# Kernel optimization log

Measured on AMD Instinct MI355X. Metric: run time of the kernel, lower is better.

Reference implementation:

```python
import jax, jax.numpy as jnp
import numpy as np

N = 50000       # nodes
E = 800000      # edges (before self loops)
F_IN = 128      # feat_dim
H = 8           # heads
C = 64          # hidden_dim (per-head out_channels, averaged since concat=False)
G = 64          # graphs in batch
NEG_SLOPE = 0.2


def setup_inputs() -> dict:
    key = jax.random.key(0)
    ks = jax.random.split(key, 16)
    inp = {
        "x": jax.random.normal(ks[0], (N, F_IN), jnp.float32),
        "edge_index": jax.random.randint(ks[1], (2, E), 0, N, dtype=jnp.int32),
        "batch": jnp.sort(jax.random.randint(ks[2], (N,), 0, G, dtype=jnp.int32)),
        "edge_attr": jax.random.normal(ks[3], (E, 4), jnp.float32),
    }
    # GATConv params per layer: lin weight [in, H*C], att_src/att_dst [H, C], bias [C]
    dims_in = [F_IN, C, C]
    for i, din in enumerate(dims_in):
        s = 1.0 / np.sqrt(din)
        inp[f"W{i}"] = jax.random.uniform(ks[4 + 3 * i], (din, H * C), jnp.float32, -s, s)
        inp[f"asrc{i}"] = jax.random.uniform(ks[5 + 3 * i], (H, C), jnp.float32, -s, s)
        inp[f"adst{i}"] = jax.random.uniform(ks[6 + 3 * i], (H, C), jnp.float32, -s, s)
        inp[f"b{i}"] = jnp.zeros((C,), jnp.float32)
    return inp


def _gat_conv(x, src, dst, W, asrc, adst, b):
    n = x.shape[0]
    h = (x @ W).reshape(n, H, C)                       # [N,H,C]
    a_s = (h * asrc[None]).sum(-1)                     # [N,H]
    a_d = (h * adst[None]).sum(-1)                     # [N,H]
    e = a_s[src] + a_d[dst]                            # [Etot,H]
    e = jnp.where(e > 0, e, NEG_SLOPE * e)             # leaky_relu(0.2)
    # segment softmax over incoming edges of each dst node (self loops => nonempty)
    m = jax.ops.segment_max(e, dst, num_segments=n)    # [N,H]
    ex = jnp.exp(e - m[dst])
    denom = jax.ops.segment_sum(ex, dst, num_segments=n)
    alpha = ex / denom[dst]                            # [Etot,H]
    out = jax.ops.segment_sum(alpha[:, :, None] * h[src], dst, num_segments=n)  # [N,H,C]
    return out.mean(axis=1) + b[None]                  # concat=False -> head mean, + bias


def reference(x, edge_index, batch, edge_attr,
              W0, asrc0, adst0, b0,
              W1, asrc1, adst1, b1,
              W2, asrc2, adst2, b2):
    # edge_attr is ignored: GATConv built without edge_dim has no lin_edge.
    loop = jnp.arange(N, dtype=edge_index.dtype)
    src = jnp.concatenate([edge_index[0], loop])       # PyG add_self_loops=True
    dst = jnp.concatenate([edge_index[1], loop])
    layers = [(W0, asrc0, adst0, b0), (W1, asrc1, adst1, b1), (W2, asrc2, adst2, b2)]
    xs = []
    h = x
    for (W, a_s, a_d, b) in layers:
        h = jax.nn.elu(_gat_conv(h, src, dst, W, a_s, a_d, b))
        xs.append(h)
    # pool='sum' -> global_add_pool per layer, then concat over layers
    pooled = [jax.ops.segment_sum(t, batch, num_segments=G) for t in xs]
    global_rep = jnp.concatenate(pooled, axis=1)       # [G, 3*C]
    return global_rep, h
```

## Files before the change

### kernel.cpp

```cpp
#include <hip/hip_runtime.h>
#include <math.h>

#define NN 50000
#define EE 800000
#define ET (EE + NN)
#define FIN 128
#define HH 8
#define CC 64
#define HC 512
#define HU 256
#define GG 64
#define POOL_SZ (GG * 3 * CC)

typedef short short8 __attribute__((ext_vector_type(8)));
typedef float floatx4 __attribute__((ext_vector_type(4)));

__device__ __forceinline__ unsigned bf16pack(float a, float b) {
    unsigned ua = __float_as_uint(a), ub = __float_as_uint(b);
    ua = (ua + 0x7FFFu + ((ua >> 16) & 1u)) >> 16;
    ub = (ub + 0x7FFFu + ((ub >> 16) & 1u)) >> 16;
    return ua | (ub << 16);
}
__device__ __forceinline__ unsigned short bf16r(float a) {
    unsigned ua = __float_as_uint(a);
    return (unsigned short)((ua + 0x7FFFu + ((ua >> 16) & 1u)) >> 16);
}
__device__ __forceinline__ float bf_lo(unsigned u) { return __uint_as_float(u << 16); }
__device__ __forceinline__ float bf_hi(unsigned u) { return __uint_as_float(u & 0xFFFF0000u); }


__global__ void k_cvt(const float* __restrict__ in, unsigned* __restrict__ out, int n8) {
    int i = blockIdx.x * blockDim.x + threadIdx.x;
    if (i < n8) {
        float4 a = ((const float4*)in)[i * 2];
        float4 b = ((const float4*)in)[i * 2 + 1];
        uint4 o;
        o.x = bf16pack(a.x, a.y); o.y = bf16pack(a.z, a.w);
        o.z = bf16pack(b.x, b.y); o.w = bf16pack(b.z, b.w);
        ((uint4*)out)[i] = o;
    }
}


__global__ void k_init(int* cnt) {
    int i = blockIdx.x * blockDim.x + threadIdx.x;
    if (i < NN) cnt[i] = 1;
}

__global__ void k_count(const int* __restrict__ dst, int* cnt) {
    int e = blockIdx.x * blockDim.x + threadIdx.x;
    if (e < EE) atomicAdd(&cnt[dst[e]], 1);
}

#define SCAN_B 256
__global__ void k_scan1(const int* __restrict__ cnt, int* off, int* bsum, int n) {
    __shared__ int s[SCAN_B];
    int i = blockIdx.x * SCAN_B + threadIdx.x;
    int v = (i < n) ? cnt[i] : 0;
    s[threadIdx.x] = v;
    __syncthreads();
    for (int d = 1; d < SCAN_B; d <<= 1) {
        int t = (threadIdx.x >= d) ? s[threadIdx.x - d] : 0;
        __syncthreads();
        s[threadIdx.x] += t;
        __syncthreads();
    }
    if (i < n) off[i] = s[threadIdx.x] - v;
    if (threadIdx.x == SCAN_B - 1) bsum[blockIdx.x] = s[SCAN_B - 1];
}

__global__ void k_scan2(int* bsum, int nb) {
    __shared__ int s[SCAN_B];
    int v = (threadIdx.x < nb) ? bsum[threadIdx.x] : 0;
    s[threadIdx.x] = v;
    __syncthreads();
    for (int d = 1; d < SCAN_B; d <<= 1) {
        int t = (threadIdx.x >= d) ? s[threadIdx.x - d] : 0;
        __syncthreads();
        s[threadIdx.x] += t;
        __syncthreads();
    }
    if (threadIdx.x < nb) bsum[threadIdx.x] = s[threadIdx.x] - v;
}

__global__ void k_scan3(int* off, const int* __restrict__ bsum, int* cursor, int n, int total) {
    int i = blockIdx.x * blockDim.x + threadIdx.x;
    if (i < n) {
        int v = off[i] + bsum[i / SCAN_B];
        off[i] = v;
        cursor[i] = v + 1;
    }
    if (i == 0) off[n] = total;
}

__global__ void k_fillself(const int* __restrict__ off, int* col) {
    int i = blockIdx.x * blockDim.x + threadIdx.x;
    if (i < NN) col[off[i]] = i;
}

__global__ void k_fill(const int* __restrict__ src, const int* __restrict__ dst,
                       int* cursor, int* col) {
    int e = blockIdx.x * blockDim.x + threadIdx.x;
    if (e < EE) {
        int p = atomicAdd(&cursor[dst[e]], 1);
        col[p] = src[e];
    }
}


template<int K>
__global__ __launch_bounds__(256) void k_gemm_mfma(
        const unsigned short* __restrict__ A,
        const float* __restrict__ W,
        const float* __restrict__ asrc, const float* __restrict__ adst,
        unsigned short* __restrict__ hout,
        float* __restrict__ as_out, float* __restrict__ ad_out, int M) {
    __shared__ unsigned short Asl[4][64][8];
    __shared__ unsigned short Bsl[4][64][8];
    const int row0 = blockIdx.x * 64;
    const int head = blockIdx.y;
    const int col0 = head * 64;
    const int tid  = threadIdx.x;
    const int w    = tid >> 6;
    const int lane = tid & 63;
    const int kgl  = lane >> 4;
    const int l15  = lane & 15;

    floatx4 acc[4] = {};

    const int kgs = tid >> 6;
    const int rc  = tid & 63;

    for (int kt = 0; kt < K; kt += 32) {
        uint4 av = make_uint4(0, 0, 0, 0);
        if (row0 + rc < M)
            av = *(const uint4*)(A + (size_t)(row0 + rc) * K + kt + kgs * 8);
        *(uint4*)&Asl[kgs][rc][0] = av;
        float wv[8];
        #pragma unroll
        for (int e = 0; e < 8; ++e)
            wv[e] = W[(size_t)(kt + kgs * 8 + e) * HC + col0 + rc];
        uint4 bv;
        bv.x = bf16pack(wv[0], wv[1]); bv.y = bf16pack(wv[2], wv[3]);
        bv.z = bf16pack(wv[4], wv[5]); bv.w = bf16pack(wv[6], wv[7]);
        *(uint4*)&Bsl[kgs][rc][0] = bv;
        __syncthreads();

        short8 af = *(const short8*)&Asl[kgl][16 * w + l15][0];
        #pragma unroll
        for (int fj = 0; fj < 4; ++fj) {
            short8 bf = *(const short8*)&Bsl[kgl][16 * fj + l15][0];
            acc[fj] = __builtin_amdgcn_mfma_f32_16x16x32_bf16(af, bf, acc[fj], 0, 0, 0);
        }
        __syncthreads();
    }

    float sav[4], dav[4];
    #pragma unroll
    for (int fj = 0; fj < 4; ++fj) {
        sav[fj] = asrc[col0 + 16 * fj + l15];
        dav[fj] = adst[col0 + 16 * fj + l15];
    }
    const int r4 = lane >> 4;
    #pragma unroll
    for (int reg = 0; reg < 4; ++reg) {
        int gr = row0 + 16 * w + r4 * 4 + reg;
        float ps = acc[0][reg] * sav[0] + acc[1][reg] * sav[1]
                 + acc[2][reg] * sav[2] + acc[3][reg] * sav[3];
        float pd = acc[0][reg] * dav[0] + acc[1][reg] * dav[1]
                 + acc[2][reg] * dav[2] + acc[3][reg] * dav[3];
        ps += __shfl_xor(ps, 1); ps += __shfl_xor(ps, 2);
        ps += __shfl_xor(ps, 4); ps += __shfl_xor(ps, 8);
        pd += __shfl_xor(pd, 1); pd += __shfl_xor(pd, 2);
        pd += __shfl_xor(pd, 4); pd += __shfl_xor(pd, 8);
        if (gr < M) {
            #pragma unroll
            for (int fj = 0; fj < 4; ++fj)
                hout[(size_t)gr * HC + col0 + 16 * fj + l15] = bf16r(acc[fj][reg]);
            if (l15 == 0) {
                as_out[gr * HH + head] = ps;
                ad_out[gr * HH + head] = pd;
            }
        }
    }
}


__global__ __launch_bounds__(256) void k_aggw(
        const unsigned* __restrict__ hb, const float* __restrict__ as,
        const float* __restrict__ ad, const int* __restrict__ off,
        const int* __restrict__ col, const float* __restrict__ bias,
        float* __restrict__ yout, unsigned* __restrict__ yb) {
    __shared__ float s_alpha[4][64][HH];
    __shared__ int   s_src[4][64];

    const int w    = threadIdx.x >> 6;
    const int lane = threadIdx.x & 63;
    const int n    = blockIdx.x * 4 + w;
    const int e0   = off[n];
    const int tot  = off[n + 1] - e0;
    const int hsel = lane >> 5;

    float adv[HH];
    {
        float4 a0 = *(const float4*)&ad[n * HH];
        float4 a1 = *(const float4*)&ad[n * HH + 4];
        adv[0] = a0.x; adv[1] = a0.y; adv[2] = a0.z; adv[3] = a0.w;
        adv[4] = a1.x; adv[5] = a1.y; adv[6] = a1.z; adv[7] = a1.w;
    }

    float d4[4] = {0.f, 0.f, 0.f, 0.f};
    float acc[8];
    #pragma unroll
    for (int i = 0; i < 8; ++i) acc[i] = 0.f;

    for (int base = 0; base < tot; base += 64) {
        const int cnt = min(64, tot - base);
        float num[HH];
        if (lane < cnt) {
            int s = col[e0 + base + lane];
            s_src[w][lane] = s;
            float4 a0 = *(const float4*)&as[s * HH];
            float4 a1 = *(const float4*)&as[s * HH + 4];
            float e[HH];
            e[0] = a0.x + adv[0]; e[1] = a0.y + adv[1];
            e[2] = a0.z + adv[2]; e[3] = a0.w + adv[3];
            e[4] = a1.x + adv[4]; e[5] = a1.y + adv[5];
            e[6] = a1.z + adv[6]; e[7] = a1.w + adv[7];
            #pragma unroll
            for (int h = 0; h < HH; ++h) {
                e[h] = e[h] > 0.f ? e[h] : 0.2f * e[h];
                num[h] = __expf(e[h]);
            }
            *(float4*)&s_alpha[w][lane][0] = make_float4(num[0], num[1], num[2], num[3]);
            *(float4*)&s_alpha[w][lane][4] = make_float4(num[4], num[5], num[6], num[7]);
        } else {
            #pragma unroll
            for (int h = 0; h < HH; ++h) num[h] = 0.f;
        }
        #pragma unroll
        for (int h = 0; h < HH; ++h) {
            float v = num[h];
            v += __shfl_xor(v, 1);  v += __shfl_xor(v, 2);
            v += __shfl_xor(v, 4);  v += __shfl_xor(v, 8);
            v += __shfl_xor(v, 16); v += __shfl_xor(v, 32);
            num[h] = v;
        }
        #pragma unroll
        for (int i = 0; i < 4; ++i) d4[i] += num[2 * i + hsel];
        #define STEP(jj) { \
            int sj = s_src[w][jj]; \
            const unsigned* _p = &hb[(size_t)sj * HU + lane]; \
            unsigned u0 = _p[0], u1 = _p[64], u2 = _p[128], u3 = _p[192]; \
            float a0 = s_alpha[w][jj][hsel]; \
            float a1 = s_alpha[w][jj][2 + hsel]; \
            float a2 = s_alpha[w][jj][4 + hsel]; \
            float a3 = s_alpha[w][jj][6 + hsel]; \
            acc[0] += a0 * bf_lo(u0); acc[1] += a0 * bf_hi(u0); \
            acc[2] += a1 * bf_lo(u1); acc[3] += a1 * bf_hi(u1); \
            acc[4] += a2 * bf_lo(u2); acc[5] += a2 * bf_hi(u2); \
            acc[6] += a3 * bf_lo(u3); acc[7] += a3 * bf_hi(u3); }
        int j = 0;
        for (; j + 4 <= cnt; j += 4) { STEP(j); STEP(j + 1); STEP(j + 2); STEP(j + 3); }
        for (; j < cnt; ++j) STEP(j);
        #undef STEP
    }

    #pragma unroll
    for (int i = 0; i < 4; ++i) {
        float r = 1.f / d4[i];
        acc[2 * i] *= r; acc[2 * i + 1] *= r;
    }
    float sx = acc[0] + acc[2] + acc[4] + acc[6];
    float sy = acc[1] + acc[3] + acc[5] + acc[7];
    sx += __shfl_xor(sx, 32);
    sy += __shfl_xor(sy, 32);
    if (lane < 32) {
        float2 bv = *(const float2*)&bias[lane * 2];
        float vx = sx * 0.125f + bv.x;
        float vy = sy * 0.125f + bv.y;
        vx = vx > 0.f ? vx : (__expf(vx) - 1.f);
        vy = vy > 0.f ? vy : (__expf(vy) - 1.f);
        *(float2*)&yout[(size_t)n * CC + lane * 2] = make_float2(vx, vy);
        yb[(size_t)n * 32 + lane] = bf16pack(vx, vy);
    }
}


__global__ __launch_bounds__(256) void k_pool(
        const float* __restrict__ y, const int* __restrict__ batch,
        float* __restrict__ pooled, int layerOff) {
    __shared__ float red[256];
    const int g = blockIdx.x;
    const int t = threadIdx.x;
    int lo = 0, hi = NN;
    while (lo < hi) { int mid = (lo + hi) >> 1; if (batch[mid] < g) lo = mid + 1; else hi = mid; }
    const int nlo = lo;
    lo = nlo; hi = NN;
    while (lo < hi) { int mid = (lo + hi) >> 1; if (batch[mid] < g + 1) lo = mid + 1; else hi = mid; }
    const int nhi = lo;

    const int c = t & 63, r = t >> 6;
    float sum = 0.f;
    for (int n = nlo + r; n < nhi; n += 4) sum += y[(size_t)n * CC + c];
    red[t] = sum;
    __syncthreads();
    if (t < 64)
        pooled[g * (3 * CC) + layerOff + t] = red[t] + red[t + 64] + red[t + 128] + red[t + 192];
}


extern "C" void kernel_launch(void* const* d_in, const int* in_sizes, int n_in,
                              void* d_out, int out_size, void* d_ws, size_t ws_size,
                              hipStream_t stream) {
    const float* x      = (const float*)d_in[0];
    const int*   ei     = (const int*)d_in[1];
    const int*   batch  = (const int*)d_in[2];
    const float* W0     = (const float*)d_in[4];
    const float* asrc0  = (const float*)d_in[5];
    const float* adst0  = (const float*)d_in[6];
    const float* b0     = (const float*)d_in[7];
    const float* W1     = (const float*)d_in[8];
    const float* asrc1  = (const float*)d_in[9];
    const float* adst1  = (const float*)d_in[10];
    const float* b1     = (const float*)d_in[11];
    const float* W2     = (const float*)d_in[12];
    const float* asrc2  = (const float*)d_in[13];
    const float* adst2  = (const float*)d_in[14];
    const float* b2     = (const float*)d_in[15];

    const int* src = ei;
    const int* dst = ei + EE;

    float* outp   = (float*)d_out;
    float* pooled = outp;
    float* hfinal = outp + POOL_SZ;

    unsigned* hb     = (unsigned*)d_ws;
    float*    y      = (float*)(hb + (size_t)NN * HU);
    float*    as_buf = y + (size_t)NN * CC;
    float*    ad_buf = as_buf + (size_t)NN * HH;
    unsigned* xb     = (unsigned*)(ad_buf + (size_t)NN * HH);
    unsigned* yb     = xb + (size_t)NN * 64;
    int*      off    = (int*)(yb + (size_t)NN * 32);
    int*      cursor = off + (NN + 1);
    int*      cnt    = cursor + NN;
    int*      col    = cnt + NN;
    int*      bsum   = col + ET;

    const int NB = (NN + SCAN_B - 1) / SCAN_B;

    k_cvt<<<(NN * FIN / 8 + 255) / 256, 256, 0, stream>>>(x, xb, NN * FIN / 8);
    k_init<<<(NN + 255) / 256, 256, 0, stream>>>(cnt);
    k_count<<<(EE + 255) / 256, 256, 0, stream>>>(dst, cnt);
    k_scan1<<<NB, SCAN_B, 0, stream>>>(cnt, off, bsum, NN);
    k_scan2<<<1, SCAN_B, 0, stream>>>(bsum, NB);
    k_scan3<<<(NN + 255) / 256, 256, 0, stream>>>(off, bsum, cursor, NN, ET);
    k_fillself<<<(NN + 255) / 256, 256, 0, stream>>>(off, col);
    k_fill<<<(EE + 255) / 256, 256, 0, stream>>>(src, dst, cursor, col);

    dim3 ggrid((NN + 63) / 64, HH);

    const float* Ws_[3]  = {W0, W1, W2};
    const float* sa_[3]  = {asrc0, asrc1, asrc2};
    const float* da_[3]  = {adst0, adst1, adst2};
    const float* bb_[3]  = {b0, b1, b2};
    float* youts[3] = {y, y, hfinal};

    for (int L = 0; L < 3; ++L) {
        if (L == 0)
            k_gemm_mfma<FIN><<<ggrid, 256, 0, stream>>>(
                (const unsigned short*)xb, Ws_[0], sa_[0], da_[0],
                (unsigned short*)hb, as_buf, ad_buf, NN);
        else
            k_gemm_mfma<CC><<<ggrid, 256, 0, stream>>>(
                (const unsigned short*)yb, Ws_[L], sa_[L], da_[L],
                (unsigned short*)hb, as_buf, ad_buf, NN);
        k_aggw<<<NN / 4, 256, 0, stream>>>(hb, as_buf, ad_buf, off, col,
                                           bb_[L], youts[L], yb);
        k_pool<<<GG, 256, 0, stream>>>(youts[L], batch, pooled, L * CC);
    }
}
```

Measured before the change: 842.1 us.

## Pre-convert weights to MFMA-fragment bf16 layout and drop LDS staging in GEMM

```diff
diff --git a/kernel.cpp b/kernel.cpp
--- a/kernel.cpp
+++ b/kernel.cpp
@@ -39,6 +39,16 @@
         o.z = bf16pack(b.x, b.y); o.w = bf16pack(b.z, b.w);
         ((uint4*)out)[i] = o;
     }
+}
+
+
+__global__ void k_wprep(const float* __restrict__ W, unsigned short* __restrict__ Wq, int KG) {
+    int g = blockIdx.x * blockDim.x + threadIdx.x;
+    if (g >= KG * 512) return;
+    int kg = g >> 9, col = g & 511;
+    #pragma unroll
+    for (int e = 0; e < 8; ++e)
+        Wq[(size_t)g * 8 + e] = bf16r(W[(size_t)(kg * 8 + e) * HC + col]);
 }
 
 
@@ -109,50 +119,34 @@
 
 
 template<int K>
-__global__ __launch_bounds__(256) void k_gemm_mfma(
+__global__ __launch_bounds__(256) void k_gemm2(
         const unsigned short* __restrict__ A,
-        const float* __restrict__ W,
+        const unsigned short* __restrict__ Wq,
         const float* __restrict__ asrc, const float* __restrict__ adst,
         unsigned short* __restrict__ hout,
         float* __restrict__ as_out, float* __restrict__ ad_out, int M) {
-    __shared__ unsigned short Asl[4][64][8];
-    __shared__ unsigned short Bsl[4][64][8];
-    const int row0 = blockIdx.x * 64;
     const int head = blockIdx.y;
     const int col0 = head * 64;
-    const int tid  = threadIdx.x;
-    const int w    = tid >> 6;
-    const int lane = tid & 63;
+    const int w    = threadIdx.x >> 6;
+    const int lane = threadIdx.x & 63;
+    const int l15  = lane & 15;
     const int kgl  = lane >> 4;
-    const int l15  = lane & 15;
+    const int row  = blockIdx.x * 64 + w * 16 + l15;
+    const bool okr = row < M;
 
     floatx4 acc[4] = {};
-
-    const int kgs = tid >> 6;
-    const int rc  = tid & 63;
-
-    for (int kt = 0; kt < K; kt += 32) {
-        uint4 av = make_uint4(0, 0, 0, 0);
-        if (row0 + rc < M)
-            av = *(const uint4*)(A + (size_t)(row0 + rc) * K + kt + kgs * 8);
-        *(uint4*)&Asl[kgs][rc][0] = av;
-        float wv[8];
-        #pragma unroll
-        for (int e = 0; e < 8; ++e)
-            wv[e] = W[(size_t)(kt + kgs * 8 + e) * HC + col0 + rc];
-        uint4 bv;
-        bv.x = bf16pack(wv[0], wv[1]); bv.y = bf16pack(wv[2], wv[3]);
-        bv.z = bf16pack(wv[4], wv[5]); bv.w = bf16pack(wv[6], wv[7]);
-        *(uint4*)&Bsl[kgs][rc][0] = bv;
-        __syncthreads();
-
-        short8 af = *(const short8*)&Asl[kgl][16 * w + l15][0];
+    const unsigned short* ap = A + (size_t)row * K + kgl * 8;
+    #pragma unroll
+    for (int kt = 0; kt < K / 32; ++kt) {
+        short8 af = {};
+        if (okr) af = *(const short8*)(ap + kt * 32);
         #pragma unroll
         for (int fj = 0; fj < 4; ++fj) {
-            short8 bf = *(const short8*)&Bsl[kgl][16 * fj + l15][0];
+            const unsigned short* bp =
+                Wq + ((size_t)((kt * 4 + kgl) * 512) + col0 + fj * 16 + l15) * 8;
+            short8 bf = *(const short8*)bp;
             acc[fj] = __builtin_amdgcn_mfma_f32_16x16x32_bf16(af, bf, acc[fj], 0, 0, 0);
         }
-        __syncthreads();
     }
 
     float sav[4], dav[4];
@@ -162,6 +156,7 @@
         dav[fj] = adst[col0 + 16 * fj + l15];
     }
     const int r4 = lane >> 4;
+    const int row0 = blockIdx.x * 64;
     #pragma unroll
     for (int reg = 0; reg < 4; ++reg) {
         int gr = row0 + 16 * w + r4 * 4 + reg;
@@ -342,7 +337,10 @@
     float*    ad_buf = as_buf + (size_t)NN * HH;
     unsigned* xb     = (unsigned*)(ad_buf + (size_t)NN * HH);
     unsigned* yb     = xb + (size_t)NN * 64;
-    int*      off    = (int*)(yb + (size_t)NN * 32);
+    unsigned short* wq0 = (unsigned short*)(yb + (size_t)NN * 32);
+    unsigned short* wq1 = wq0 + (size_t)16 * 512 * 8;
+    unsigned short* wq2 = wq1 + (size_t)8 * 512 * 8;
+    int*      off    = (int*)(wq2 + (size_t)8 * 512 * 8);
     int*      cursor = off + (NN + 1);
     int*      cnt    = cursor + NN;
     int*      col    = cnt + NN;
@@ -351,6 +349,9 @@
     const int NB = (NN + SCAN_B - 1) / SCAN_B;
 
     k_cvt<<<(NN * FIN / 8 + 255) / 256, 256, 0, stream>>>(x, xb, NN * FIN / 8);
+    k_wprep<<<(16 * 512 + 255) / 256, 256, 0, stream>>>(W0, wq0, 16);
+    k_wprep<<<(8 * 512 + 255) / 256, 256, 0, stream>>>(W1, wq1, 8);
+    k_wprep<<<(8 * 512 + 255) / 256, 256, 0, stream>>>(W2, wq2, 8);
     k_init<<<(NN + 255) / 256, 256, 0, stream>>>(cnt);
     k_count<<<(EE + 255) / 256, 256, 0, stream>>>(dst, cnt);
     k_scan1<<<NB, SCAN_B, 0, stream>>>(cnt, off, bsum, NN);
@@ -361,7 +362,7 @@
 
     dim3 ggrid((NN + 63) / 64, HH);
 
-    const float* Ws_[3]  = {W0, W1, W2};
+    const unsigned short* wqs[3] = {wq0, wq1, wq2};
     const float* sa_[3]  = {asrc0, asrc1, asrc2};
     const float* da_[3]  = {adst0, adst1, adst2};
     const float* bb_[3]  = {b0, b1, b2};
@@ -369,12 +370,12 @@
 
     for (int L = 0; L < 3; ++L) {
         if (L == 0)
-            k_gemm_mfma<FIN><<<ggrid, 256, 0, stream>>>(
-                (const unsigned short*)xb, Ws_[0], sa_[0], da_[0],
+            k_gemm2<FIN><<<ggrid, 256, 0, stream>>>(
+                (const unsigned short*)xb, wqs[0], sa_[0], da_[0],
                 (unsigned short*)hb, as_buf, ad_buf, NN);
         else
-            k_gemm_mfma<CC><<<ggrid, 256, 0, stream>>>(
-                (const unsigned short*)yb, Ws_[L], sa_[L], da_[L],
+            k_gemm2<CC><<<ggrid, 256, 0, stream>>>(
+                (const unsigned short*)yb, wqs[L], sa_[L], da_[L],
                 (unsigned short*)hb, as_buf, ad_buf, NN);
         k_aggw<<<NN / 4, 256, 0, stream>>>(hb, as_buf, ad_buf, off, col,
                                            bb_[L], youts[L], yb);
```

Measured after the change: 859.0 us. 1.02x slower.

## Split aggregation across two waves per node and fuse CSR build kernels

Applied to the files above, without the earlier changes.

```diff
diff --git a/kernel.cpp b/kernel.cpp
--- a/kernel.cpp
+++ b/kernel.cpp
@@ -29,9 +29,9 @@
 __device__ __forceinline__ float bf_hi(unsigned u) { return __uint_as_float(u & 0xFFFF0000u); }
 
 
-__global__ void k_cvt(const float* __restrict__ in, unsigned* __restrict__ out, int n8) {
+__global__ void k_prep(const float* __restrict__ in, unsigned* __restrict__ out, int* cnt) {
     int i = blockIdx.x * blockDim.x + threadIdx.x;
-    if (i < n8) {
+    if (i < NN * FIN / 8) {
         float4 a = ((const float4*)in)[i * 2];
         float4 b = ((const float4*)in)[i * 2 + 1];
         uint4 o;
@@ -39,63 +39,44 @@
         o.z = bf16pack(b.x, b.y); o.w = bf16pack(b.z, b.w);
         ((uint4*)out)[i] = o;
     }
-}
-
-
-__global__ void k_init(int* cnt) {
-    int i = blockIdx.x * blockDim.x + threadIdx.x;
     if (i < NN) cnt[i] = 1;
 }
+
 
 __global__ void k_count(const int* __restrict__ dst, int* cnt) {
     int e = blockIdx.x * blockDim.x + threadIdx.x;
     if (e < EE) atomicAdd(&cnt[dst[e]], 1);
 }
 
-#define SCAN_B 256
-__global__ void k_scan1(const int* __restrict__ cnt, int* off, int* bsum, int n) {
-    __shared__ int s[SCAN_B];
-    int i = blockIdx.x * SCAN_B + threadIdx.x;
-    int v = (i < n) ? cnt[i] : 0;
-    s[threadIdx.x] = v;
+__global__ __launch_bounds__(1024) void k_scanall(
+        const int* __restrict__ cnt, int* __restrict__ off,
+        int* __restrict__ cursor, int* __restrict__ col) {
+    __shared__ int s[1024];
+    const int t = threadIdx.x;
+    const int CPT = (NN + 1023) / 1024;
+    int base = t * CPT;
+    int lim = NN - base;
+    if (lim < 0) lim = 0;
+    if (lim > CPT) lim = CPT;
+    int sum = 0;
+    for (int i = 0; i < lim; ++i) sum += cnt[base + i];
+    s[t] = sum;
     __syncthreads();
-    for (int d = 1; d < SCAN_B; d <<= 1) {
-        int t = (threadIdx.x >= d) ? s[threadIdx.x - d] : 0;
+    for (int d = 1; d < 1024; d <<= 1) {
+        int v = (t >= d) ? s[t - d] : 0;
         __syncthreads();
-        s[threadIdx.x] += t;
+        s[t] += v;
         __syncthreads();
     }
-    if (i < n) off[i] = s[threadIdx.x] - v;
-    if (threadIdx.x == SCAN_B - 1) bsum[blockIdx.x] = s[SCAN_B - 1];
-}
-
-__global__ void k_scan2(int* bsum, int nb) {
-    __shared__ int s[SCAN_B];
-    int v = (threadIdx.x < nb) ? bsum[threadIdx.x] : 0;
-    s[threadIdx.x] = v;
-    __syncthreads();
-    for (int d = 1; d < SCAN_B; d <<= 1) {
-        int t = (threadIdx.x >= d) ? s[threadIdx.x - d] : 0;
-        __syncthreads();
-        s[threadIdx.x] += t;
-        __syncthreads();
-    }
-    if (threadIdx.x < nb) bsum[threadIdx.x] = s[threadIdx.x] - v;
-}
-
-__global__ void k_scan3(int* off, const int* __restrict__ bsum, int* cursor, int n, int total) {
-    int i = blockIdx.x * blockDim.x + threadIdx.x;
-    if (i < n) {
-        int v = off[i] + bsum[i / SCAN_B];
-        off[i] = v;
-        cursor[i] = v + 1;
-    }
-    if (i == 0) off[n] = total;
-}
-
-__global__ void k_fillself(const int* __restrict__ off, int* col) {
-    int i = blockIdx.x * blockDim.x + threadIdx.x;
-    if (i < NN) col[off[i]] = i;
+    int run = s[t] - sum;
+    for (int i = 0; i < lim; ++i) {
+        int c = cnt[base + i];
+        off[base + i] = run;
+        cursor[base + i] = run + 1;
+        col[run] = base + i;
+        run += c;
+    }
+    if (t == 0) off[NN] = ET;
 }
 
 __global__ void k_fill(const int* __restrict__ src, const int* __restrict__ dst,
@@ -191,94 +172,75 @@
         const float* __restrict__ ad, const int* __restrict__ off,
         const int* __restrict__ col, const float* __restrict__ bias,
         float* __restrict__ yout, unsigned* __restrict__ yb) {
-    __shared__ float s_alpha[4][64][HH];
-    __shared__ int   s_src[4][64];
-
-    const int w    = threadIdx.x >> 6;
+    __shared__ float s_alpha[2][2][64][4];
+    __shared__ int   s_src[2][2][64];
+    __shared__ float2 s_red[2][32];
+
+    const int wv   = (threadIdx.x >> 6) & 1;
+    const int nd   = threadIdx.x >> 7;
     const int lane = threadIdx.x & 63;
-    const int n    = blockIdx.x * 4 + w;
+    const int n    = blockIdx.x * 2 + nd;
     const int e0   = off[n];
     const int tot  = off[n + 1] - e0;
     const int hsel = lane >> 5;
 
-    float adv[HH];
-    {
-        float4 a0 = *(const float4*)&ad[n * HH];
-        float4 a1 = *(const float4*)&ad[n * HH + 4];
-        adv[0] = a0.x; adv[1] = a0.y; adv[2] = a0.z; adv[3] = a0.w;
-        adv[4] = a1.x; adv[5] = a1.y; adv[6] = a1.z; adv[7] = a1.w;
-    }
-
-    float d4[4] = {0.f, 0.f, 0.f, 0.f};
-    float acc[8];
-    #pragma unroll
-    for (int i = 0; i < 8; ++i) acc[i] = 0.f;
+    float4 adv = *(const float4*)&ad[n * HH + 4 * wv];
+
+    float d0 = 0.f, d1 = 0.f;
+    float acc[4] = {0.f, 0.f, 0.f, 0.f};
 
     for (int base = 0; base < tot; base += 64) {
         const int cnt = min(64, tot - base);
-        float num[HH];
+        float n0, n1, n2, n3;
         if (lane < cnt) {
             int s = col[e0 + base + lane];
-            s_src[w][lane] = s;
-            float4 a0 = *(const float4*)&as[s * HH];
-            float4 a1 = *(const float4*)&as[s * HH + 4];
-            float e[HH];
-            e[0] = a0.x + adv[0]; e[1] = a0.y + adv[1];
-            e[2] = a0.z + adv[2]; e[3] = a0.w + adv[3];
-            e[4] = a1.x + adv[4]; e[5] = a1.y + adv[5];
-            e[6] = a1.z + adv[6]; e[7] = a1.w + adv[7];
-            #pragma unroll
-            for (int h = 0; h < HH; ++h) {
-                e[h] = e[h] > 0.f ? e[h] : 0.2f * e[h];
-                num[h] = __expf(e[h]);
-            }
-            *(float4*)&s_alpha[w][lane][0] = make_float4(num[0], num[1], num[2], num[3]);
-            *(float4*)&s_alpha[w][lane][4] = make_float4(num[4], num[5], num[6], num[7]);
+            s_src[nd][wv][lane] = s;
+            float4 a = *(const float4*)&as[s * HH + 4 * wv];
+            float e0v = a.x + adv.x, e1v = a.y + adv.y;
+            float e2v = a.z + adv.z, e3v = a.w + adv.w;
+            e0v = e0v > 0.f ? e0v : 0.2f * e0v;
+            e1v = e1v > 0.f ? e1v : 0.2f * e1v;
+            e2v = e2v > 0.f ? e2v : 0.2f * e2v;
+            e3v = e3v > 0.f ? e3v : 0.2f * e3v;
+            n0 = __expf(e0v); n1 = __expf(e1v);
+            n2 = __expf(e2v); n3 = __expf(e3v);
+            *(float4*)&s_alpha[nd][wv][lane][0] = make_float4(n0, n1, n2, n3);
         } else {
-            #pragma unroll
-            for (int h = 0; h < HH; ++h) num[h] = 0.f;
+            n0 = n1 = n2 = n3 = 0.f;
         }
-        #pragma unroll
-        for (int h = 0; h < HH; ++h) {
-            float v = num[h];
-            v += __shfl_xor(v, 1);  v += __shfl_xor(v, 2);
-            v += __shfl_xor(v, 4);  v += __shfl_xor(v, 8);
-            v += __shfl_xor(v, 16); v += __shfl_xor(v, 32);
-            num[h] = v;
-        }
-        #pragma unroll
-        for (int i = 0; i < 4; ++i) d4[i] += num[2 * i + hsel];
+        #define RED(v) { v += __shfl_xor(v, 1);  v += __shfl_xor(v, 2); \
+                         v += __shfl_xor(v, 4);  v += __shfl_xor(v, 8); \
+                         v += __shfl_xor(v, 16); v += __shfl_xor(v, 32); }
+        RED(n0); RED(n1); RED(n2); RED(n3);
+        #undef RED
+        d0 += hsel ? n1 : n0;
+        d1 += hsel ? n3 : n2;
         #define STEP(jj) { \
-            int sj = s_src[w][jj]; \
-            const unsigned* _p = &hb[(size_t)sj * HU + lane]; \
-            unsigned u0 = _p[0], u1 = _p[64], u2 = _p[128], u3 = _p[192]; \
-            float a0 = s_alpha[w][jj][hsel]; \
-            float a1 = s_alpha[w][jj][2 + hsel]; \
-            float a2 = s_alpha[w][jj][4 + hsel]; \
-            float a3 = s_alpha[w][jj][6 + hsel]; \
+            int sj = s_src[nd][wv][jj]; \
+            const unsigned* _p = &hb[(size_t)sj * HU + wv * 128 + lane]; \
+            unsigned u0 = _p[0], u1 = _p[64]; \
+            float a0 = s_alpha[nd][wv][jj][hsel]; \
+            float a1 = s_alpha[nd][wv][jj][2 + hsel]; \
             acc[0] += a0 * bf_lo(u0); acc[1] += a0 * bf_hi(u0); \
-            acc[2] += a1 * bf_lo(u1); acc[3] += a1 * bf_hi(u1); \
-            acc[4] += a2 * bf_lo(u2); acc[5] += a2 * bf_hi(u2); \
-            acc[6] += a3 * bf_lo(u3); acc[7] += a3 * bf_hi(u3); }
+            acc[2] += a1 * bf_lo(u1); acc[3] += a1 * bf_hi(u1); }
         int j = 0;
         for (; j + 4 <= cnt; j += 4) { STEP(j); STEP(j + 1); STEP(j + 2); STEP(j + 3); }
         for (; j < cnt; ++j) STEP(j);
         #undef STEP
     }
 
-    #pragma unroll
-    for (int i = 0; i < 4; ++i) {
-        float r = 1.f / d4[i];
-        acc[2 * i] *= r; acc[2 * i + 1] *= r;
-    }
-    float sx = acc[0] + acc[2] + acc[4] + acc[6];
-    float sy = acc[1] + acc[3] + acc[5] + acc[7];
+    float r0 = 1.f / d0, r1 = 1.f / d1;
+    float sx = acc[0] * r0 + acc[2] * r1;
+    float sy = acc[1] * r0 + acc[3] * r1;
     sx += __shfl_xor(sx, 32);
     sy += __shfl_xor(sy, 32);
-    if (lane < 32) {
+    if (wv == 1 && lane < 32) s_red[nd][lane] = make_float2(sx, sy);
+    __syncthreads();
+    if (wv == 0 && lane < 32) {
+        float2 o = s_red[nd][lane];
         float2 bv = *(const float2*)&bias[lane * 2];
-        float vx = sx * 0.125f + bv.x;
-        float vy = sy * 0.125f + bv.y;
+        float vx = (sx + o.x) * 0.125f + bv.x;
+        float vy = (sy + o.y) * 0.125f + bv.y;
         vx = vx > 0.f ? vx : (__expf(vx) - 1.f);
         vy = vy > 0.f ? vy : (__expf(vy) - 1.f);
         *(float2*)&yout[(size_t)n * CC + lane * 2] = make_float2(vx, vy);
@@ -346,17 +308,10 @@
     int*      cursor = off + (NN + 1);
     int*      cnt    = cursor + NN;
     int*      col    = cnt + NN;
-    int*      bsum   = col + ET;
-
-    const int NB = (NN + SCAN_B - 1) / SCAN_B;
-
-    k_cvt<<<(NN * FIN / 8 + 255) / 256, 256, 0, stream>>>(x, xb, NN * FIN / 8);
-    k_init<<<(NN + 255) / 256, 256, 0, stream>>>(cnt);
+
+    k_prep<<<(NN * FIN / 8 + 255) / 256, 256, 0, stream>>>(x, xb, cnt);
     k_count<<<(EE + 255) / 256, 256, 0, stream>>>(dst, cnt);
-    k_scan1<<<NB, SCAN_B, 0, stream>>>(cnt, off, bsum, NN);
-    k_scan2<<<1, SCAN_B, 0, stream>>>(bsum, NB);
-    k_scan3<<<(NN + 255) / 256, 256, 0, stream>>>(off, bsum, cursor, NN, ET);
-    k_fillself<<<(NN + 255) / 256, 256, 0, stream>>>(off, col);
+    k_scanall<<<1, 1024, 0, stream>>>(cnt, off, cursor, col);
     k_fill<<<(EE + 255) / 256, 256, 0, stream>>>(src, dst, cursor, col);
 
     dim3 ggrid((NN + 63) / 64, HH);
@@ -376,7 +331,7 @@
             k_gemm_mfma<CC><<<ggrid, 256, 0, stream>>>(
                 (const unsigned short*)yb, Ws_[L], sa_[L], da_[L],
                 (unsigned short*)hb, as_buf, ad_buf, NN);
-        k_aggw<<<NN / 4, 256, 0, stream>>>(hb, as_buf, ad_buf, off, col,
+        k_aggw<<<NN / 2, 256, 0, stream>>>(hb, as_buf, ad_buf, off, col,
                                            bb_[L], youts[L], yb);
         k_pool<<<GG, 256, 0, stream>>>(youts[L], batch, pooled, L * CC);
     }
```

Result: slower. 959.2 us (+13.9%).
